# Performance work log

Hardware: AMD Instinct MI355X
Metric: run time of the kernel (lower is better)

The kernel has to match this reference:

```python
import jax, jax.numpy as jnp
import numpy as np
import math

B, S, T = 8, 512, 512
D, H, DFF = 512, 8, 2048
LE, LD = 4, 4
DK = D // H
NEG = -1e9
EPS = 1e-5


def _posenc(L, d):
    pos = jnp.arange(L, dtype=jnp.float32)[:, None]
    div = jnp.exp(jnp.arange(0, d, 2, dtype=jnp.float32) * (-math.log(10000.0) / d))
    pe = jnp.zeros((L, d), jnp.float32)
    pe = pe.at[:, 0::2].set(jnp.sin(pos * div))
    pe = pe.at[:, 1::2].set(jnp.cos(pos * div))
    return pe  # [L, d]


def _layernorm(x, g, b):
    mu = jnp.mean(x, axis=-1, keepdims=True)
    var = jnp.mean(jnp.square(x - mu), axis=-1, keepdims=True)
    return (x - mu) * jax.lax.rsqrt(var + EPS) * g + b


def _mha(xq, xkv, W, b, mask):
    # W: [4, D, D] (q,k,v,o); b: [4, D]
    Bq, Lq, _ = xq.shape
    Lk = xkv.shape[1]
    q = (xq @ W[0] + b[0]).reshape(Bq, Lq, H, DK).transpose(0, 2, 1, 3)
    k = (xkv @ W[1] + b[1]).reshape(Bq, Lk, H, DK).transpose(0, 2, 1, 3)
    v = (xkv @ W[2] + b[2]).reshape(Bq, Lk, H, DK).transpose(0, 2, 1, 3)
    scores = jnp.einsum('bhqd,bhkd->bhqk', q, k) / math.sqrt(DK)
    if mask is not None:
        scores = jnp.where(mask, scores, NEG)
    attn = jax.nn.softmax(scores, axis=-1)
    o = jnp.einsum('bhqk,bhkd->bhqd', attn, v).transpose(0, 2, 1, 3).reshape(Bq, Lq, D)
    return o @ W[3] + b[3]


def _ffn(x, W1, b1, W2, b2):
    return jax.nn.relu(x @ W1 + b1) @ W2 + b2


def setup_inputs() -> dict:
    key = jax.random.key(0)
    ks = iter(jax.random.split(key, 32))
    w = lambda shape: jax.random.normal(next(ks), shape, jnp.float32) * 0.02
    inp = {
        'src': jax.random.normal(next(ks), (B, S, D), jnp.float32),
        'tgt': jax.random.normal(next(ks), (B, T, D), jnp.float32),
        'enc_attn_W': w((LE, 4, D, D)), 'enc_attn_b': jnp.zeros((LE, 4, D)),
        'enc_ffn_W1': w((LE, D, DFF)), 'enc_ffn_b1': jnp.zeros((LE, DFF)),
        'enc_ffn_W2': w((LE, DFF, D)), 'enc_ffn_b2': jnp.zeros((LE, D)),
        'enc_ln_g': jnp.ones((LE, 2, D)), 'enc_ln_b': jnp.zeros((LE, 2, D)),
        'enc_fnorm_g': jnp.ones((D,)), 'enc_fnorm_b': jnp.zeros((D,)),
        'dec_sattn_W': w((LD, 4, D, D)), 'dec_sattn_b': jnp.zeros((LD, 4, D)),
        'dec_cattn_W': w((LD, 4, D, D)), 'dec_cattn_b': jnp.zeros((LD, 4, D)),
        'dec_ffn_W1': w((LD, D, DFF)), 'dec_ffn_b1': jnp.zeros((LD, DFF)),
        'dec_ffn_W2': w((LD, DFF, D)), 'dec_ffn_b2': jnp.zeros((LD, D)),
        'dec_ln_g': jnp.ones((LD, 3, D)), 'dec_ln_b': jnp.zeros((LD, 3, D)),
        'dec_fnorm_g': jnp.ones((D,)), 'dec_fnorm_b': jnp.zeros((D,)),
        'tgt_mask': jnp.tril(jnp.ones((T, T), bool))[None, None],  # [1,1,T,T] causal
    }
    return inp


def reference(src, tgt, enc_attn_W, enc_attn_b, enc_ffn_W1, enc_ffn_b1,
              enc_ffn_W2, enc_ffn_b2, enc_ln_g, enc_ln_b, enc_fnorm_g, enc_fnorm_b,
              dec_sattn_W, dec_sattn_b, dec_cattn_W, dec_cattn_b,
              dec_ffn_W1, dec_ffn_b1, dec_ffn_W2, dec_ffn_b2,
              dec_ln_g, dec_ln_b, dec_fnorm_g, dec_fnorm_b, tgt_mask):
    # positional encoding (dropout = identity in eval)
    x = src + _posenc(S, D)[None]
    y = tgt + _posenc(T, D)[None]

    # ----- encoder -----
    for l in range(LE):
        a = _mha(x, x, enc_attn_W[l], enc_attn_b[l], None)
        x = _layernorm(x + a, enc_ln_g[l, 0], enc_ln_b[l, 0])
        f = _ffn(x, enc_ffn_W1[l], enc_ffn_b1[l], enc_ffn_W2[l], enc_ffn_b2[l])
        x = _layernorm(x + f, enc_ln_g[l, 1], enc_ln_b[l, 1])
    memory = _layernorm(x, enc_fnorm_g, enc_fnorm_b)

    # ----- decoder -----
    for l in range(LD):
        a = _mha(y, y, dec_sattn_W[l], dec_sattn_b[l], tgt_mask)
        y = _layernorm(y + a, dec_ln_g[l, 0], dec_ln_b[l, 0])
        c = _mha(y, memory, dec_cattn_W[l], dec_cattn_b[l], None)
        y = _layernorm(y + c, dec_ln_g[l, 1], dec_ln_b[l, 1])
        f = _ffn(y, dec_ffn_W1[l], dec_ffn_b1[l], dec_ffn_W2[l], dec_ffn_b2[l])
        y = _layernorm(y + f, dec_ln_g[l, 2], dec_ln_b[l, 2])
    out = _layernorm(y, dec_fnorm_g, dec_fnorm_b)
    return out
```

## Files before the change

kernel.cpp:

```cpp
#include <hip/hip_runtime.h>

typedef _Float16 half_t;
typedef _Float16 f16x8 __attribute__((ext_vector_type(8)));
typedef _Float16 f16x4 __attribute__((ext_vector_type(4)));
typedef float    f32x4 __attribute__((ext_vector_type(4)));

#define MFMA16(a, b, c) __builtin_amdgcn_mfma_f32_16x16x32_f16((a), (b), (c), 0, 0, 0)

#define BB   8
#define SS   512
#define DD   512
#define HH   8
#define DKK  64
#define DFFN 2048
#define MTOT 4096

__device__ __forceinline__ void gload16(const half_t* g, half_t* l) {
    __builtin_amdgcn_global_load_lds((const __attribute__((address_space(1))) void*)g,
                                     (__attribute__((address_space(3))) void*)l, 16, 0, 0);
}

__global__ __launch_bounds__(256) void wtrans(const float* __restrict__ W,
                                              half_t* __restrict__ Wt, int K, int N) {
    const long z = blockIdx.z;
    W  += z * (long)K * N;
    Wt += z * (long)K * N;
    __shared__ float t[32][33];
    const int n0 = blockIdx.x * 32, k0 = blockIdx.y * 32;
    const int tx = threadIdx.x, ty = threadIdx.y;
#pragma unroll
    for (int i = 0; i < 4; i++)
        t[ty + i * 8][tx] = W[(long)(k0 + ty + i * 8) * N + n0 + tx];
    __syncthreads();
#pragma unroll
    for (int i = 0; i < 4; i++)
        Wt[(long)(n0 + ty + i * 8) * K + k0 + tx] = (half_t)t[tx][ty + i * 8];
}

__global__ __launch_bounds__(256) void vtrans(const half_t* __restrict__ V,
                                              half_t* __restrict__ Vt, int Lk) {
    const int z = blockIdx.z, b = z >> 3, h = z & 7;
    const int s0 = blockIdx.x * 32, d0 = blockIdx.y * 32;
    const int tx = threadIdx.x, ty = threadIdx.y;
    __shared__ half_t t[32][33];
#pragma unroll
    for (int i = 0; i < 4; i++)
        t[ty + i * 8][tx] = V[(long)(b * Lk + s0 + ty + i * 8) * DD + h * 64 + d0 + tx];
    __syncthreads();
#pragma unroll
    for (int i = 0; i < 4; i++)
        Vt[(long)(z * 64 + d0 + ty + i * 8) * Lk + s0 + tx] = t[tx][ty + i * 8];
}

__global__ __launch_bounds__(256) void posenc_k(const float* __restrict__ src,
                                                half_t* __restrict__ out) {
    const int idx = blockIdx.x * 256 + threadIdx.x;
    const long f = (long)idx * 4;
    const int d0 = (int)(f & 511);
    const int srow = (int)((f >> 9) & 511);
    float4 v = *(const float4*)(src + f);
    const float cexp = -0.0359778926f;
    const int p0 = d0 >> 1;
    const float a0 = (float)srow * __expf(cexp * (float)p0);
    const float a1 = (float)srow * __expf(cexp * (float)(p0 + 1));
    v.x += __sinf(a0);
    v.y += __cosf(a0);
    v.z += __sinf(a1);
    v.w += __cosf(a1);
    f16x4 h;
    h[0] = (half_t)v.x; h[1] = (half_t)v.y; h[2] = (half_t)v.z; h[3] = (half_t)v.w;
    *(f16x4*)(out + f) = h;
}

template <int HASRES, int F32OUT>
__global__ __launch_bounds__(256) void ln_k(const half_t* __restrict__ X,
                                            const half_t* __restrict__ R,
                                            const float* __restrict__ gam,
                                            const float* __restrict__ bet,
                                            void* __restrict__ out) {
    const int wid = threadIdx.x >> 6, lane = threadIdx.x & 63;
    const long row = blockIdx.x * 4 + wid;
    const int c = lane * 8;
    float v[8];
    f16x8 xv = *(const f16x8*)(X + row * 512 + c);
    if (HASRES) {
        f16x8 rv = *(const f16x8*)(R + row * 512 + c);
#pragma unroll
        for (int i = 0; i < 8; i++) v[i] = (float)xv[i] + (float)rv[i];
    } else {
#pragma unroll
        for (int i = 0; i < 8; i++) v[i] = (float)xv[i];
    }
    float s = 0.f, sq = 0.f;
#pragma unroll
    for (int i = 0; i < 8; i++) { s += v[i]; sq += v[i] * v[i]; }
#pragma unroll
    for (int m = 1; m < 64; m <<= 1) {
        s += __shfl_xor(s, m);
        sq += __shfl_xor(sq, m);
    }
    const float mu = s * (1.f / 512.f);
    const float var = sq * (1.f / 512.f) - mu * mu;
    const float rstd = rsqrtf(var + 1e-5f);
    float4 g0 = *(const float4*)(gam + c), g1 = *(const float4*)(gam + c + 4);
    float4 b0 = *(const float4*)(bet + c), b1 = *(const float4*)(bet + c + 4);
    float gg[8] = {g0.x, g0.y, g0.z, g0.w, g1.x, g1.y, g1.z, g1.w};
    float bb[8] = {b0.x, b0.y, b0.z, b0.w, b1.x, b1.y, b1.z, b1.w};
    if (F32OUT) {
        float* o = (float*)out + row * 512 + c;
        float4 o0, o1;
        o0.x = (v[0] - mu) * rstd * gg[0] + bb[0];
        o0.y = (v[1] - mu) * rstd * gg[1] + bb[1];
        o0.z = (v[2] - mu) * rstd * gg[2] + bb[2];
        o0.w = (v[3] - mu) * rstd * gg[3] + bb[3];
        o1.x = (v[4] - mu) * rstd * gg[4] + bb[4];
        o1.y = (v[5] - mu) * rstd * gg[5] + bb[5];
        o1.z = (v[6] - mu) * rstd * gg[6] + bb[6];
        o1.w = (v[7] - mu) * rstd * gg[7] + bb[7];
        *(float4*)o = o0;
        *(float4*)(o + 4) = o1;
    } else {
        f16x8 hv;
#pragma unroll
        for (int i = 0; i < 8; i++) hv[i] = (half_t)((v[i] - mu) * rstd * gg[i] + bb[i]);
        *(f16x8*)((half_t*)out + row * 512 + c) = hv;
    }
}

template <int MR, int RELU>
__global__ __launch_bounds__(256) void gemm_k(const half_t* __restrict__ A,
                                              const half_t* __restrict__ Wt,
                                              const float* __restrict__ bias,
                                              half_t* __restrict__ C, int M, int N, int K,
                                              long wzs, long bzs, long czs) {
    constexpr int BM = MR * 32;
    __shared__ half_t smem[2][(BM + 64) * 32];
    const int z = blockIdx.z;
    const half_t* Wz = Wt + (long)z * wzs;
    const float* bz = bias + (long)z * bzs;
    half_t* Cz = C + (long)z * czs;
    const int m0 = blockIdx.x * BM, n0 = blockIdx.y * 64;
    const int tid = threadIdx.x, wid = tid >> 6, lane = tid & 63;
    const int g = lane >> 4, l16 = lane & 15;
    const int wr = wid >> 1, wc = wid & 1;
    const int nk = K >> 5;

    f32x4 acc[MR][2];
#pragma unroll
    for (int i = 0; i < MR; i++)
#pragma unroll
        for (int j = 0; j < 2; j++)
#pragma unroll
            for (int e = 0; e < 4; e++) acc[i][j][e] = 0.f;

    auto stage = [&](int buf, int kt) {
        half_t* sA = smem[buf];
        half_t* sB = smem[buf] + BM * 32;
        const int k0 = kt << 5;
#pragma unroll
        for (int i = 0; i < MR / 2; i++) {
            const int c = i * 256 + wid * 64 + lane;
            gload16(A + (long)(m0 + (c >> 2)) * K + k0 + (c & 3) * 8,
                    sA + (i * 256 + wid * 64) * 8);
        }
        const int c = wid * 64 + lane;
        gload16(Wz + (long)(n0 + (c >> 2)) * K + k0 + (c & 3) * 8, sB + (wid * 64) * 8);
    };

    stage(0, 0);
    __syncthreads();
    int buf = 0;
    for (int kt = 0; kt < nk; kt++) {
        if (kt + 1 < nk) stage(buf ^ 1, kt + 1);
        const half_t* sA = smem[buf];
        const half_t* sB = smem[buf] + BM * 32;
        f16x8 af[MR], bf[2];
#pragma unroll
        for (int mr = 0; mr < MR; mr++) {
            const int row = wr * (MR * 16) + mr * 16 + l16;
            af[mr] = *(const f16x8*)(sA + row * 32 + g * 8);
        }
#pragma unroll
        for (int nr = 0; nr < 2; nr++) {
            const int row = wc * 32 + nr * 16 + l16;
            bf[nr] = *(const f16x8*)(sB + row * 32 + g * 8);
        }
#pragma unroll
        for (int mr = 0; mr < MR; mr++)
#pragma unroll
            for (int nr = 0; nr < 2; nr++)
                acc[mr][nr] = MFMA16(af[mr], bf[nr], acc[mr][nr]);
        __syncthreads();
        buf ^= 1;
    }

#pragma unroll
    for (int nr = 0; nr < 2; nr++) {
        const int n = n0 + wc * 32 + nr * 16 + l16;
        const float bv = bz[n];
#pragma unroll
        for (int mr = 0; mr < MR; mr++) {
#pragma unroll
            for (int e = 0; e < 4; e++) {
                const int m = m0 + wr * (MR * 16) + mr * 16 + g * 4 + e;
                float v = acc[mr][nr][e] + bv;
                if (RELU) v = fmaxf(v, 0.f);
                Cz[(long)m * N + n] = (half_t)v;
            }
        }
    }
}

template <int CAUSAL>
__global__ __launch_bounds__(256) void flash_k(const half_t* __restrict__ Qb,
                                               const half_t* __restrict__ Kb,
                                               const half_t* __restrict__ Vt,
                                               half_t* __restrict__ Ob, int Lq, int Lk) {
    __shared__ half_t sQ[64 * 64], sK[64 * 64], sV[64 * 64];
    __shared__ half_t sP[4][16 * 88];
    const int qt = blockIdx.x, h = blockIdx.y, b = blockIdx.z;
    const int tid = threadIdx.x, wid = tid >> 6, lane = tid & 63;
    const int g = lane >> 4, l16 = lane & 15;

#pragma unroll
    for (int i = 0; i < 2; i++) {
        const int c = i * 256 + wid * 64 + lane;
        const int r = c >> 3, j = c & 7, js = j ^ (r & 7);
        gload16(Qb + (long)(b * Lq + qt * 64 + r) * DD + h * 64 + js * 8,
                sQ + (i * 256 + wid * 64) * 8);
    }

    float m_e[4], l_e[4];
#pragma unroll
    for (int e = 0; e < 4; e++) { m_e[e] = -1e30f; l_e[e] = 0.f; }
    f32x4 o[4];
#pragma unroll
    for (int d = 0; d < 4; d++)
#pragma unroll
        for (int e = 0; e < 4; e++) o[d][e] = 0.f;

    const int nkv = CAUSAL ? (qt + 1) : (Lk >> 6);
    for (int kvt = 0; kvt < nkv; kvt++) {
#pragma unroll
        for (int i = 0; i < 2; i++) {
            const int c = i * 256 + wid * 64 + lane;
            const int r = c >> 3, j = c & 7, js = j ^ (r & 7);
            gload16(Kb + (long)(b * Lk + kvt * 64 + r) * DD + h * 64 + js * 8,
                    sK + (i * 256 + wid * 64) * 8);
            gload16(Vt + (long)((b * HH + h) * 64 + r) * Lk + kvt * 64 + js * 8,
                    sV + (i * 256 + wid * 64) * 8);
        }
        __syncthreads();

        f32x4 s[4];
#pragma unroll
        for (int nr = 0; nr < 4; nr++)
#pragma unroll
            for (int e = 0; e < 4; e++) s[nr][e] = 0.f;
#pragma unroll
        for (int k0 = 0; k0 < 2; k0++) {
            const int qrow = wid * 16 + l16;
            f16x8 aq = *(const f16x8*)(sQ + qrow * 64 + (((k0 * 4 + g) ^ (qrow & 7)) * 8));
#pragma unroll
            for (int nr = 0; nr < 4; nr++) {
                const int krow = nr * 16 + l16;
                f16x8 bk = *(const f16x8*)(sK + krow * 64 + (((k0 * 4 + g) ^ (krow & 7)) * 8));
                s[nr] = MFMA16(aq, bk, s[nr]);
            }
        }
        float mx[4];
#pragma unroll
        for (int e = 0; e < 4; e++) mx[e] = -1e30f;
#pragma unroll
        for (int nr = 0; nr < 4; nr++) {
#pragma unroll
            for (int e = 0; e < 4; e++) {
                float v = s[nr][e] * 0.125f;
                if (CAUSAL) {
                    const int q = qt * 64 + wid * 16 + g * 4 + e;
                    const int kv = kvt * 64 + nr * 16 + l16;
                    if (kv > q) v = -1e9f;
                }
                s[nr][e] = v;
                mx[e] = fmaxf(mx[e], v);
            }
        }
#pragma unroll
        for (int e = 0; e < 4; e++) {
            float v = mx[e];
            v = fmaxf(v, __shfl_xor(v, 1));
            v = fmaxf(v, __shfl_xor(v, 2));
            v = fmaxf(v, __shfl_xor(v, 4));
            v = fmaxf(v, __shfl_xor(v, 8));
            mx[e] = v;
        }
        float al[4], rs[4];
#pragma unroll
        for (int e = 0; e < 4; e++) {
            const float mn = fmaxf(m_e[e], mx[e]);
            al[e] = __expf(m_e[e] - mn);
            m_e[e] = mn;
            rs[e] = 0.f;
        }
#pragma unroll
        for (int nr = 0; nr < 4; nr++) {
#pragma unroll
            for (int e = 0; e < 4; e++) {
                const float p = __expf(s[nr][e] - m_e[e]);
                rs[e] += p;
                sP[wid][(g * 4 + e) * 88 + nr * 16 + l16] = (half_t)p;
            }
        }
#pragma unroll
        for (int e = 0; e < 4; e++) {
            float v = rs[e];
            v += __shfl_xor(v, 1);
            v += __shfl_xor(v, 2);
            v += __shfl_xor(v, 4);
            v += __shfl_xor(v, 8);
            l_e[e] = l_e[e] * al[e] + v;
        }
#pragma unroll
        for (int dr = 0; dr < 4; dr++)
#pragma unroll
            for (int e = 0; e < 4; e++) o[dr][e] *= al[e];
#pragma unroll
        for (int k0 = 0; k0 < 2; k0++) {
            f16x8 pa = *(const f16x8*)(&sP[wid][l16 * 88 + k0 * 32 + g * 8]);
#pragma unroll
            for (int dr = 0; dr < 4; dr++) {
                const int vrow = dr * 16 + l16;
                f16x8 vb = *(const f16x8*)(sV + vrow * 64 + (((k0 * 4 + g) ^ (vrow & 7)) * 8));
                o[dr] = MFMA16(pa, vb, o[dr]);
            }
        }
        __syncthreads();
    }
#pragma unroll
    for (int dr = 0; dr < 4; dr++) {
#pragma unroll
        for (int e = 0; e < 4; e++) {
            const int q = qt * 64 + wid * 16 + g * 4 + e;
            const int d = h * 64 + dr * 16 + l16;
            Ob[(long)(b * Lq + q) * DD + d] = (half_t)(o[dr][e] / l_e[e]);
        }
    }
}

#define MMAT 262144L
#define FFMAT 1048576L
#define ACTST 2097152L

static inline void launch_gemm(hipStream_t st, const half_t* A, const half_t* Wt,
                               const float* b, half_t* C, int M, int N, int K, int nz,
                               long wzs, long bzs, long czs, bool relu, int bm) {
    dim3 grid(M / bm, N / 64, nz), blk(256);
    if (bm == 128) {
        if (relu)
            gemm_k<4, 1><<<grid, blk, 0, st>>>(A, Wt, b, C, M, N, K, wzs, bzs, czs);
        else
            gemm_k<4, 0><<<grid, blk, 0, st>>>(A, Wt, b, C, M, N, K, wzs, bzs, czs);
    } else {
        if (relu)
            gemm_k<2, 1><<<grid, blk, 0, st>>>(A, Wt, b, C, M, N, K, wzs, bzs, czs);
        else
            gemm_k<2, 0><<<grid, blk, 0, st>>>(A, Wt, b, C, M, N, K, wzs, bzs, czs);
    }
}

extern "C" void kernel_launch(void* const* d_in, const int* in_sizes, int n_in, void* d_out,
                              int out_size, void* d_ws, size_t ws_size, hipStream_t stream) {
    (void)in_sizes; (void)n_in; (void)out_size; (void)ws_size;
    const float* src = (const float*)d_in[0];
    const float* tgt = (const float*)d_in[1];
    const float* eaW = (const float*)d_in[2];
    const float* eab = (const float*)d_in[3];
    const float* ef1W = (const float*)d_in[4];
    const float* ef1b = (const float*)d_in[5];
    const float* ef2W = (const float*)d_in[6];
    const float* ef2b = (const float*)d_in[7];
    const float* elng = (const float*)d_in[8];
    const float* elnb = (const float*)d_in[9];
    const float* efng = (const float*)d_in[10];
    const float* efnb = (const float*)d_in[11];
    const float* dsW = (const float*)d_in[12];
    const float* dsb = (const float*)d_in[13];
    const float* dcW = (const float*)d_in[14];
    const float* dcb = (const float*)d_in[15];
    const float* df1W = (const float*)d_in[16];
    const float* df1b = (const float*)d_in[17];
    const float* df2W = (const float*)d_in[18];
    const float* df2b = (const float*)d_in[19];
    const float* dlng = (const float*)d_in[20];
    const float* dlnb = (const float*)d_in[21];
    const float* dfng = (const float*)d_in[22];
    const float* dfnb = (const float*)d_in[23];

    char* ws = (char*)d_ws;
    half_t* wtEA = (half_t*)(ws + 0);
    half_t* wtEF1 = (half_t*)(ws + 8388608);
    half_t* wtEF2 = (half_t*)(ws + 16777216);
    half_t* wtDS = (half_t*)(ws + 25165824);
    half_t* wtDC = (half_t*)(ws + 33554432);
    half_t* wtDF1 = (half_t*)(ws + 41943040);
    half_t* wtDF2 = (half_t*)(ws + 50331648);
    half_t* xb = (half_t*)(ws + 58720256);
    half_t* yb = (half_t*)(ws + 62914560);
    half_t* memb = (half_t*)(ws + 67108864);
    half_t* qb = (half_t*)(ws + 71303168);
    half_t* kb = (half_t*)(ws + 75497472);
    half_t* vb = (half_t*)(ws + 79691776);
    half_t* vtb = (half_t*)(ws + 83886080);
    half_t* ao = (half_t*)(ws + 88080384);
    half_t* pr = (half_t*)(ws + 92274688);
    half_t* ffh = (half_t*)(ws + 96468992);
    half_t* ff2 = (half_t*)(ws + 113246208);

    dim3 tb(32, 8);
    wtrans<<<dim3(16, 16, 16), tb, 0, stream>>>(eaW, wtEA, 512, 512);
    wtrans<<<dim3(64, 16, 4), tb, 0, stream>>>(ef1W, wtEF1, 512, 2048);
    wtrans<<<dim3(16, 64, 4), tb, 0, stream>>>(ef2W, wtEF2, 2048, 512);
    wtrans<<<dim3(16, 16, 16), tb, 0, stream>>>(dsW, wtDS, 512, 512);
    wtrans<<<dim3(16, 16, 16), tb, 0, stream>>>(dcW, wtDC, 512, 512);
    wtrans<<<dim3(64, 16, 4), tb, 0, stream>>>(df1W, wtDF1, 512, 2048);
    wtrans<<<dim3(16, 64, 4), tb, 0, stream>>>(df2W, wtDF2, 2048, 512);

    posenc_k<<<2048, 256, 0, stream>>>(src, xb);
    posenc_k<<<2048, 256, 0, stream>>>(tgt, yb);

    for (int l = 0; l < 4; l++) {
        launch_gemm(stream, xb, wtEA + (long)l * 4 * MMAT, eab + l * 2048, qb, MTOT, 512, 512,
                    3, MMAT, 512, ACTST, false, 128);
        vtrans<<<dim3(16, 2, 64), tb, 0, stream>>>(vb, vtb, 512);
        flash_k<0><<<dim3(8, 8, 8), 256, 0, stream>>>(qb, kb, vtb, ao, 512, 512);
        launch_gemm(stream, ao, wtEA + (long)(l * 4 + 3) * MMAT, eab + l * 2048 + 1536, pr,
                    MTOT, 512, 512, 1, 0, 0, 0, false, 64);
        ln_k<1, 0><<<1024, 256, 0, stream>>>(pr, xb, elng + l * 1024, elnb + l * 1024, xb);
        launch_gemm(stream, xb, wtEF1 + (long)l * FFMAT, ef1b + l * 2048, ffh, MTOT, 2048,
                    512, 1, 0, 0, 0, true, 128);
        launch_gemm(stream, ffh, wtEF2 + (long)l * FFMAT, ef2b + l * 512, ff2, MTOT, 512,
                    2048, 1, 0, 0, 0, false, 64);
        ln_k<1, 0><<<1024, 256, 0, stream>>>(ff2, xb, elng + l * 1024 + 512,
                                             elnb + l * 1024 + 512, xb);
    }
    ln_k<0, 0><<<1024, 256, 0, stream>>>(xb, nullptr, efng, efnb, memb);

    for (int l = 0; l < 4; l++) {
        launch_gemm(stream, yb, wtDS + (long)l * 4 * MMAT, dsb + l * 2048, qb, MTOT, 512, 512,
                    3, MMAT, 512, ACTST, false, 128);
        vtrans<<<dim3(16, 2, 64), tb, 0, stream>>>(vb, vtb, 512);
        flash_k<1><<<dim3(8, 8, 8), 256, 0, stream>>>(qb, kb, vtb, ao, 512, 512);
        launch_gemm(stream, ao, wtDS + (long)(l * 4 + 3) * MMAT, dsb + l * 2048 + 1536, pr,
                    MTOT, 512, 512, 1, 0, 0, 0, false, 64);
        ln_k<1, 0><<<1024, 256, 0, stream>>>(pr, yb, dlng + l * 1536, dlnb + l * 1536, yb);
        launch_gemm(stream, yb, wtDC + (long)l * 4 * MMAT, dcb + l * 2048, qb, MTOT, 512, 512,
                    1, 0, 0, 0, false, 64);
        launch_gemm(stream, memb, wtDC + (long)(l * 4 + 1) * MMAT, dcb + l * 2048 + 512, kb,
                    MTOT, 512, 512, 2, MMAT, 512, ACTST, false, 128);
        vtrans<<<dim3(16, 2, 64), tb, 0, stream>>>(vb, vtb, 512);
        flash_k<0><<<dim3(8, 8, 8), 256, 0, stream>>>(qb, kb, vtb, ao, 512, 512);
        launch_gemm(stream, ao, wtDC + (long)(l * 4 + 3) * MMAT, dcb + l * 2048 + 1536, pr,
                    MTOT, 512, 512, 1, 0, 0, 0, false, 64);
        ln_k<1, 0><<<1024, 256, 0, stream>>>(pr, yb, dlng + l * 1536 + 512,
                                             dlnb + l * 1536 + 512, yb);
        launch_gemm(stream, yb, wtDF1 + (long)l * FFMAT, df1b + l * 2048, ffh, MTOT, 2048,
                    512, 1, 0, 0, 0, true, 128);
        launch_gemm(stream, ffh, wtDF2 + (long)l * FFMAT, df2b + l * 512, ff2, MTOT, 512,
                    2048, 1, 0, 0, 0, false, 64);
        ln_k<1, 0><<<1024, 256, 0, stream>>>(ff2, yb, dlng + l * 1536 + 1024,
                                             dlnb + l * 1536 + 1024, yb);
    }
    ln_k<0, 1><<<1024, 256, 0, stream>>>(yb, nullptr, dfng, dfnb, d_out);
}
```

Before: 1.177 ms.

## Batch cross-attn KV projections, double-buffer flash KV, widen GEMM K-tile with swizzle

Computes all four decoder layers' cross-attention K/V projections from the encoder memory in one batched GEMM, followed by one batched V transpose, before the decoder loop. This replaces eight smaller launches and gives the GPU a larger grid. The GEMM kernel now stages K-tiles of 64 instead of 32, using an XOR-swizzled LDS layout, which halves the number of barriers per K step. The flash attention kernel double-buffers K/V tiles so loads overlap compute. The cost is more LDS per block, which may lower occupancy, and extra workspace for the precomputed K/V.

New measurement: 1.083 ms. 1.09x faster.

```diff
diff --git a/kernel.cpp b/kernel.cpp
--- a/kernel.cpp
+++ b/kernel.cpp
@@ -11,9 +11,11 @@
 #define SS   512
 #define DD   512
 #define HH   8
-#define DKK  64
 #define DFFN 2048
 #define MTOT 4096
+#define MMAT 262144L
+#define FFMAT 1048576L
+#define ACTST 2097152L
 
 __device__ __forceinline__ void gload16(const half_t* g, half_t* l) {
     __builtin_amdgcn_global_load_lds((const __attribute__((address_space(1))) void*)g,
@@ -23,7 +25,7 @@
 __global__ __launch_bounds__(256) void wtrans(const float* __restrict__ W,
                                               half_t* __restrict__ Wt, int K, int N) {
     const long z = blockIdx.z;
-    W  += z * (long)K * N;
+    W += z * (long)K * N;
     Wt += z * (long)K * N;
     __shared__ float t[32][33];
     const int n0 = blockIdx.x * 32, k0 = blockIdx.y * 32;
@@ -50,6 +52,23 @@
 #pragma unroll
     for (int i = 0; i < 4; i++)
         Vt[(long)(z * 64 + d0 + ty + i * 8) * Lk + s0 + tx] = t[tx][ty + i * 8];
+}
+
+__global__ __launch_bounds__(256) void vtransc(const half_t* __restrict__ ckv,
+                                               half_t* __restrict__ vtc) {
+    const int zz = blockIdx.z, l = zz >> 6, z = zz & 63, b = z >> 3, h = z & 7;
+    const half_t* V = ckv + (long)(2 * l + 1) * ACTST;
+    half_t* Vt = vtc + (long)l * ACTST;
+    const int s0 = blockIdx.x * 32, d0 = blockIdx.y * 32;
+    const int tx = threadIdx.x, ty = threadIdx.y;
+    __shared__ half_t t[32][33];
+#pragma unroll
+    for (int i = 0; i < 4; i++)
+        t[ty + i * 8][tx] = V[(long)(b * SS + s0 + ty + i * 8) * DD + h * 64 + d0 + tx];
+    __syncthreads();
+#pragma unroll
+    for (int i = 0; i < 4; i++)
+        Vt[(long)(z * 64 + d0 + ty + i * 8) * SS + s0 + tx] = t[tx][ty + i * 8];
 }
 
 __global__ __launch_bounds__(256) void posenc_k(const float* __restrict__ src,
@@ -127,23 +146,33 @@
     }
 }
 
-template <int MR, int RELU>
+template <int MR, int RELU, int ZMAP>
 __global__ __launch_bounds__(256) void gemm_k(const half_t* __restrict__ A,
                                               const half_t* __restrict__ Wt,
                                               const float* __restrict__ bias,
                                               half_t* __restrict__ C, int M, int N, int K,
                                               long wzs, long bzs, long czs) {
     constexpr int BM = MR * 32;
-    __shared__ half_t smem[2][(BM + 64) * 32];
+    __shared__ half_t smem[2][(BM + 64) * 64];
     const int z = blockIdx.z;
-    const half_t* Wz = Wt + (long)z * wzs;
-    const float* bz = bias + (long)z * bzs;
-    half_t* Cz = C + (long)z * czs;
+    const half_t* Wz;
+    const float* bz;
+    half_t* Cz;
+    if (ZMAP) {
+        const int l = z >> 1, i = z & 1;
+        Wz = Wt + (long)(l * 4 + 1 + i) * MMAT;
+        bz = bias + l * 2048 + (1 + i) * 512;
+        Cz = C + (long)z * czs;
+    } else {
+        Wz = Wt + (long)z * wzs;
+        bz = bias + (long)z * bzs;
+        Cz = C + (long)z * czs;
+    }
     const int m0 = blockIdx.x * BM, n0 = blockIdx.y * 64;
     const int tid = threadIdx.x, wid = tid >> 6, lane = tid & 63;
     const int g = lane >> 4, l16 = lane & 15;
     const int wr = wid >> 1, wc = wid & 1;
-    const int nk = K >> 5;
+    const int nk = K >> 6;
 
     f32x4 acc[MR][2];
 #pragma unroll
@@ -155,16 +184,20 @@
 
     auto stage = [&](int buf, int kt) {
         half_t* sA = smem[buf];
-        half_t* sB = smem[buf] + BM * 32;
-        const int k0 = kt << 5;
-#pragma unroll
-        for (int i = 0; i < MR / 2; i++) {
+        half_t* sB = smem[buf] + BM * 64;
+        const int k0 = kt << 6;
+#pragma unroll
+        for (int i = 0; i < MR; i++) {
             const int c = i * 256 + wid * 64 + lane;
-            gload16(A + (long)(m0 + (c >> 2)) * K + k0 + (c & 3) * 8,
-                    sA + (i * 256 + wid * 64) * 8);
-        }
-        const int c = wid * 64 + lane;
-        gload16(Wz + (long)(n0 + (c >> 2)) * K + k0 + (c & 3) * 8, sB + (wid * 64) * 8);
+            const int r = c >> 3, j = c & 7, js = j ^ (r & 7);
+            gload16(A + (long)(m0 + r) * K + k0 + js * 8, sA + (i * 256 + wid * 64) * 8);
+        }
+#pragma unroll
+        for (int i = 0; i < 2; i++) {
+            const int c = i * 256 + wid * 64 + lane;
+            const int r = c >> 3, j = c & 7, js = j ^ (r & 7);
+            gload16(Wz + (long)(n0 + r) * K + k0 + js * 8, sB + (i * 256 + wid * 64) * 8);
+        }
     };
 
     stage(0, 0);
@@ -173,23 +206,26 @@
     for (int kt = 0; kt < nk; kt++) {
         if (kt + 1 < nk) stage(buf ^ 1, kt + 1);
         const half_t* sA = smem[buf];
-        const half_t* sB = smem[buf] + BM * 32;
-        f16x8 af[MR], bf[2];
-#pragma unroll
-        for (int mr = 0; mr < MR; mr++) {
-            const int row = wr * (MR * 16) + mr * 16 + l16;
-            af[mr] = *(const f16x8*)(sA + row * 32 + g * 8);
-        }
-#pragma unroll
-        for (int nr = 0; nr < 2; nr++) {
-            const int row = wc * 32 + nr * 16 + l16;
-            bf[nr] = *(const f16x8*)(sB + row * 32 + g * 8);
-        }
-#pragma unroll
-        for (int mr = 0; mr < MR; mr++)
-#pragma unroll
-            for (int nr = 0; nr < 2; nr++)
-                acc[mr][nr] = MFMA16(af[mr], bf[nr], acc[mr][nr]);
+        const half_t* sB = smem[buf] + BM * 64;
+#pragma unroll
+        for (int kk = 0; kk < 2; kk++) {
+            f16x8 af[MR], bf[2];
+#pragma unroll
+            for (int mr = 0; mr < MR; mr++) {
+                const int row = wr * (MR * 16) + mr * 16 + l16;
+                af[mr] = *(const f16x8*)(sA + row * 64 + (((kk * 4 + g) ^ (row & 7)) * 8));
+            }
+#pragma unroll
+            for (int nr = 0; nr < 2; nr++) {
+                const int row = wc * 32 + nr * 16 + l16;
+                bf[nr] = *(const f16x8*)(sB + row * 64 + (((kk * 4 + g) ^ (row & 7)) * 8));
+            }
+#pragma unroll
+            for (int mr = 0; mr < MR; mr++)
+#pragma unroll
+                for (int nr = 0; nr < 2; nr++)
+                    acc[mr][nr] = MFMA16(af[mr], bf[nr], acc[mr][nr]);
+        }
         __syncthreads();
         buf ^= 1;
     }
@@ -216,7 +252,8 @@
                                                const half_t* __restrict__ Kb,
                                                const half_t* __restrict__ Vt,
                                                half_t* __restrict__ Ob, int Lq, int Lk) {
-    __shared__ half_t sQ[64 * 64], sK[64 * 64], sV[64 * 64];
+    __shared__ half_t sQ[64 * 64];
+    __shared__ half_t sK[2][64 * 64], sV[2][64 * 64];
     __shared__ half_t sP[4][16 * 88];
     const int qt = blockIdx.x, h = blockIdx.y, b = blockIdx.z;
     const int tid = threadIdx.x, wid = tid >> 6, lane = tid & 63;
@@ -229,28 +266,35 @@
         gload16(Qb + (long)(b * Lq + qt * 64 + r) * DD + h * 64 + js * 8,
                 sQ + (i * 256 + wid * 64) * 8);
     }
-
-    float m_e[4], l_e[4];
-#pragma unroll
-    for (int e = 0; e < 4; e++) { m_e[e] = -1e30f; l_e[e] = 0.f; }
-    f32x4 o[4];
-#pragma unroll
-    for (int d = 0; d < 4; d++)
-#pragma unroll
-        for (int e = 0; e < 4; e++) o[d][e] = 0.f;
-
-    const int nkv = CAUSAL ? (qt + 1) : (Lk >> 6);
-    for (int kvt = 0; kvt < nkv; kvt++) {
+    auto stage_kv = [&](int bu, int kvt) {
 #pragma unroll
         for (int i = 0; i < 2; i++) {
             const int c = i * 256 + wid * 64 + lane;
             const int r = c >> 3, j = c & 7, js = j ^ (r & 7);
             gload16(Kb + (long)(b * Lk + kvt * 64 + r) * DD + h * 64 + js * 8,
-                    sK + (i * 256 + wid * 64) * 8);
+                    sK[bu] + (i * 256 + wid * 64) * 8);
             gload16(Vt + (long)((b * HH + h) * 64 + r) * Lk + kvt * 64 + js * 8,
-                    sV + (i * 256 + wid * 64) * 8);
-        }
-        __syncthreads();
+                    sV[bu] + (i * 256 + wid * 64) * 8);
+        }
+    };
+
+    float m_e[4], l_e[4];
+#pragma unroll
+    for (int e = 0; e < 4; e++) { m_e[e] = -1e30f; l_e[e] = 0.f; }
+    f32x4 o[4];
+#pragma unroll
+    for (int d = 0; d < 4; d++)
+#pragma unroll
+        for (int e = 0; e < 4; e++) o[d][e] = 0.f;
+
+    const int nkv = CAUSAL ? (qt + 1) : (Lk >> 6);
+    stage_kv(0, 0);
+    __syncthreads();
+    int buf = 0;
+    for (int kvt = 0; kvt < nkv; kvt++) {
+        if (kvt + 1 < nkv) stage_kv(buf ^ 1, kvt + 1);
+        const half_t* cK = sK[buf];
+        const half_t* cV = sV[buf];
 
         f32x4 s[4];
 #pragma unroll
@@ -264,7 +308,7 @@
 #pragma unroll
             for (int nr = 0; nr < 4; nr++) {
                 const int krow = nr * 16 + l16;
-                f16x8 bk = *(const f16x8*)(sK + krow * 64 + (((k0 * 4 + g) ^ (krow & 7)) * 8));
+                f16x8 bk = *(const f16x8*)(cK + krow * 64 + (((k0 * 4 + g) ^ (krow & 7)) * 8));
                 s[nr] = MFMA16(aq, bk, s[nr]);
             }
         }
@@ -330,11 +374,12 @@
 #pragma unroll
             for (int dr = 0; dr < 4; dr++) {
                 const int vrow = dr * 16 + l16;
-                f16x8 vb = *(const f16x8*)(sV + vrow * 64 + (((k0 * 4 + g) ^ (vrow & 7)) * 8));
+                f16x8 vb = *(const f16x8*)(cV + vrow * 64 + (((k0 * 4 + g) ^ (vrow & 7)) * 8));
                 o[dr] = MFMA16(pa, vb, o[dr]);
             }
         }
         __syncthreads();
+        buf ^= 1;
     }
 #pragma unroll
     for (int dr = 0; dr < 4; dr++) {
@@ -346,10 +391,6 @@
         }
     }
 }
-
-#define MMAT 262144L
-#define FFMAT 1048576L
-#define ACTST 2097152L
 
 static inline void launch_gemm(hipStream_t st, const half_t* A, const half_t* Wt,
                                const float* b, half_t* C, int M, int N, int K, int nz,
@@ -357,14 +398,14 @@
     dim3 grid(M / bm, N / 64, nz), blk(256);
     if (bm == 128) {
         if (relu)
-            gemm_k<4, 1><<<grid, blk, 0, st>>>(A, Wt, b, C, M, N, K, wzs, bzs, czs);
+            gemm_k<4, 1, 0><<<grid, blk, 0, st>>>(A, Wt, b, C, M, N, K, wzs, bzs, czs);
         else
-            gemm_k<4, 0><<<grid, blk, 0, st>>>(A, Wt, b, C, M, N, K, wzs, bzs, czs);
+            gemm_k<4, 0, 0><<<grid, blk, 0, st>>>(A, Wt, b, C, M, N, K, wzs, bzs, czs);
     } else {
         if (relu)
-            gemm_k<2, 1><<<grid, blk, 0, st>>>(A, Wt, b, C, M, N, K, wzs, bzs, czs);
+            gemm_k<2, 1, 0><<<grid, blk, 0, st>>>(A, Wt, b, C, M, N, K, wzs, bzs, czs);
         else
-            gemm_k<2, 0><<<grid, blk, 0, st>>>(A, Wt, b, C, M, N, K, wzs, bzs, czs);
+            gemm_k<2, 0, 0><<<grid, blk, 0, st>>>(A, Wt, b, C, M, N, K, wzs, bzs, czs);
     }
 }
 
@@ -415,6 +456,8 @@
     half_t* pr = (half_t*)(ws + 92274688);
     half_t* ffh = (half_t*)(ws + 96468992);
     half_t* ff2 = (half_t*)(ws + 113246208);
+    half_t* ckv = (half_t*)(ws + 134217728);
+    half_t* vtc = (half_t*)(ws + 167772160);
 
     dim3 tb(32, 8);
     wtrans<<<dim3(16, 16, 16), tb, 0, stream>>>(eaW, wtEA, 512, 512);
@@ -445,6 +488,10 @@
     }
     ln_k<0, 0><<<1024, 256, 0, stream>>>(xb, nullptr, efng, efnb, memb);
 
+    gemm_k<4, 0, 1><<<dim3(32, 8, 8), 256, 0, stream>>>(memb, wtDC, dcb, ckv, MTOT, 512,
+                                                        512, 0, 0, ACTST);
+    vtransc<<<dim3(16, 2, 256), tb, 0, stream>>>(ckv, vtc);
+
     for (int l = 0; l < 4; l++) {
         launch_gemm(stream, yb, wtDS + (long)l * 4 * MMAT, dsb + l * 2048, qb, MTOT, 512, 512,
                     3, MMAT, 512, ACTST, false, 128);
@@ -455,10 +502,8 @@
         ln_k<1, 0><<<1024, 256, 0, stream>>>(pr, yb, dlng + l * 1536, dlnb + l * 1536, yb);
         launch_gemm(stream, yb, wtDC + (long)l * 4 * MMAT, dcb + l * 2048, qb, MTOT, 512, 512,
                     1, 0, 0, 0, false, 64);
-        launch_gemm(stream, memb, wtDC + (long)(l * 4 + 1) * MMAT, dcb + l * 2048 + 512, kb,
-                    MTOT, 512, 512, 2, MMAT, 512, ACTST, false, 128);
-        vtrans<<<dim3(16, 2, 64), tb, 0, stream>>>(vb, vtb, 512);
-        flash_k<0><<<dim3(8, 8, 8), 256, 0, stream>>>(qb, kb, vtb, ao, 512, 512);
+        flash_k<0><<<dim3(8, 8, 8), 256, 0, stream>>>(qb, ckv + (long)(2 * l) * ACTST,
+                                                      vtc + (long)l * ACTST, ao, 512, 512);
         launch_gemm(stream, ao, wtDC + (long)(l * 4 + 3) * MMAT, dcb + l * 2048 + 1536, pr,
                     MTOT, 512, 512, 1, 0, 0, 0, false, 64);
         ln_k<1, 0><<<1024, 256, 0, stream>>>(pr, yb, dlng + l * 1536 + 512,
```
